# Kernel tuning notes

Measured on AMD Instinct MI355X. Metric: run time of the kernel, lower is better.

The kernel has to match this reference:

```python
import jax, jax.numpy as jnp
import numpy as np
from jax.scipy.special import ndtri

BLOCK_SIZE = 32
NF5_OFFSET = 0.9677083  # QLoRA-style tail quantile offset


def _nf5_table():
    # 32-level NormalFloat-5 table: 16 negative levels, zero, 15 positive levels,
    # taken from standard-normal quantiles and normalized so endpoints hit -1 / +1.
    neg = ndtri(jnp.linspace(1.0 - NF5_OFFSET, 0.5, 17))[:-1]   # 16 negative quantiles
    pos = ndtri(jnp.linspace(0.5, NF5_OFFSET, 16))[1:]          # 15 positive quantiles
    neg = neg / (-neg[0])
    pos = pos / pos[-1]
    return jnp.concatenate([neg, jnp.zeros((1,)), pos]).astype(jnp.float32)


def nf5_quantize(x, block_size, table, boundaries):
    # Block-wise NF5 quantization with power-of-2 scales along the last dim.
    shp = x.shape
    xb = x.reshape(-1, block_size)                               # [nblocks, B]
    amax = jnp.max(jnp.abs(xb), axis=1, keepdims=True)
    scale = jnp.exp2(jnp.ceil(jnp.log2(jnp.maximum(amax, 1e-12))))  # power-of-2 scale
    n = xb / scale                                               # normalized to [-1, 1]
    idx = jnp.searchsorted(boundaries, n)                        # nearest-level index
    q = table[idx] * scale                                       # fused dequant
    return q.reshape(shp)


def setup_inputs() -> dict:
    key = jax.random.key(0)
    k1, k2, k3 = jax.random.split(key, 3)
    B, S, Din, Dout = 8, 4096, 1024, 1024
    x = jax.random.normal(k1, (B, S, Din), dtype=jnp.float32)
    # kaiming_uniform_(a=sqrt(5)) -> U(-b, b) with b = sqrt(6/((1+5)*fan_in)) = 1/sqrt(fan_in)
    bound_w = 1.0 / np.sqrt(Din)
    weight = jax.random.uniform(k2, (Dout, Din), minval=-bound_w, maxval=bound_w, dtype=jnp.float32)
    bias = jax.random.uniform(k3, (Dout,), minval=-bound_w, maxval=bound_w, dtype=jnp.float32)
    return {"x": x, "weight": weight, "bias": bias}


def reference(x, weight, bias):
    table = _nf5_table()
    boundaries = (table[:-1] + table[1:]) * 0.5
    qw = nf5_quantize(weight, BLOCK_SIZE, table, boundaries)   # quantize weight along in_features
    qx = nf5_quantize(x, BLOCK_SIZE, table, boundaries)        # quantize_input=True
    # y[b,s,o] = sum_k qx[b,s,k] * qw[o,k] + bias[o]
    y = jnp.einsum('bsk,ok->bso', qx, qw) + bias
    return y
```

## Files before the change

### kernel.cpp

```cpp
#include <hip/hip_runtime.h>
#include <hip/hip_bf16.h>

typedef __attribute__((ext_vector_type(8))) short short8;
typedef __attribute__((ext_vector_type(4))) float f32x4;

struct alignas(8) US4 { unsigned short x, y, z, w; };

__device__ double ndtri_d(double p) {
    const double a1 = -3.969683028665376e+01, a2 = 2.209460984245205e+02,
                 a3 = -2.759285104469687e+02, a4 = 1.383577518672690e+02,
                 a5 = -3.066479806614716e+01, a6 = 2.506628277459239e+00;
    const double b1 = -5.447609879822406e+01, b2 = 1.615858368580409e+02,
                 b3 = -1.556989798598866e+02, b4 = 6.680131188771972e+01,
                 b5 = -1.328068155288572e+01;
    const double c1 = -7.784894002430293e-03, c2 = -3.223964580411365e-01,
                 c3 = -2.400758277161838e+00, c4 = -2.549732539343734e+00,
                 c5 = 4.374664141464968e+00,  c6 = 2.938163982698783e+00;
    const double d1 = 7.784695709041462e-03, d2 = 3.224671290700398e-01,
                 d3 = 2.445134137142996e+00, d4 = 3.754408661907416e+00;
    const double plow = 0.02425, phigh = 1.0 - 0.02425;
    double x;
    if (p < plow) {
        double q = sqrt(-2.0 * log(p));
        x = (((((c1*q+c2)*q+c3)*q+c4)*q+c5)*q+c6) / ((((d1*q+d2)*q+d3)*q+d4)*q+1.0);
    } else if (p <= phigh) {
        double q = p - 0.5, r = q * q;
        x = (((((a1*r+a2)*r+a3)*r+a4)*r+a5)*r+a6)*q / (((((b1*r+b2)*r+b3)*r+b4)*r+b5)*r+1.0);
    } else {
        double q = sqrt(-2.0 * log(1.0 - p));
        x = -(((((c1*q+c2)*q+c3)*q+c4)*q+c5)*q+c6) / ((((d1*q+d2)*q+d3)*q+d4)*q+1.0);
    }
    #pragma unroll
    for (int it = 0; it < 2; ++it) {
        double e = 0.5 * erfc(-x * 0.70710678118654752440) - p;
        double u = e * 2.50662827463100050242 * exp(0.5 * x * x);
        x = x - u / (1.0 + 0.5 * x * u);
    }
    return x;
}

__global__ void build_table_k(float* __restrict__ table, float* __restrict__ bounds) {
    __shared__ float sT[32];
    const int i = threadIdx.x;
    const double OFF = 0.9677083;
    double v;
    if (i == 16) {
        v = 0.0;
    } else if (i < 16) {
        const double a = 1.0 - OFF;
        double p = a + (0.5 - a) * ((double)i / 16.0);
        v = ndtri_d(p) / (-ndtri_d(a));
    } else {
        int j = i - 16;
        double p = 0.5 + (OFF - 0.5) * ((double)j / 15.0);
        v = ndtri_d(p) / ndtri_d(OFF);
    }
    float tv = (float)v;
    sT[i] = tv;
    table[i] = tv;
    __syncthreads();
    if (i < 31) bounds[i] = 0.5f * (sT[i] + sT[i + 1]);
    else        bounds[31] = __builtin_inff();
}

__device__ __forceinline__ unsigned short q_one(float n, const float* sT,
                                                const float* sB, float scale) {
    int idx = (sB[15] < n) ? 16 : 0;
    idx += (sB[idx + 7] < n) ? 8 : 0;
    idx += (sB[idx + 3] < n) ? 4 : 0;
    idx += (sB[idx + 1] < n) ? 2 : 0;
    idx += (sB[idx]     < n) ? 1 : 0;
    float q = sT[idx] * scale;
    __hip_bfloat16 h = __float2bfloat16(q);
    return *reinterpret_cast<unsigned short*>(&h);
}

__global__ __launch_bounds__(256) void quantize_k(const float4* __restrict__ in,
                                                  US4* __restrict__ out,
                                                  const float* __restrict__ table,
                                                  const float* __restrict__ bounds,
                                                  int n4) {
    __shared__ float sT[32], sB[32];
    const int tid = threadIdx.x;
    if (tid < 32) { sT[tid] = table[tid]; sB[tid] = bounds[tid]; }
    __syncthreads();
    const int t = blockIdx.x * 256 + tid;
    if (t >= n4) return;
    float4 v = in[t];
    float am = fmaxf(fmaxf(fabsf(v.x), fabsf(v.y)), fmaxf(fabsf(v.z), fabsf(v.w)));
    am = fmaxf(am, __shfl_xor(am, 1));
    am = fmaxf(am, __shfl_xor(am, 2));
    am = fmaxf(am, __shfl_xor(am, 4));
    am = fmaxf(am, 1e-12f);
    int e;
    float m = frexpf(am, &e);
    int se = (m == 0.5f) ? (e - 1) : e;
    float scale = ldexpf(1.0f, se);
    float inv   = ldexpf(1.0f, -se);
    US4 o;
    o.x = q_one(v.x * inv, sT, sB, scale);
    o.y = q_one(v.y * inv, sT, sB, scale);
    o.z = q_one(v.z * inv, sT, sB, scale);
    o.w = q_one(v.w * inv, sT, sB, scale);
    out[t] = o;
}

__device__ __forceinline__ void gload_lds16(const unsigned short* g, unsigned short* s) {
    __builtin_amdgcn_global_load_lds(
        (const __attribute__((address_space(1))) unsigned int*)g,
        (__attribute__((address_space(3))) unsigned int*)s, 16, 0, 0);
}

__global__ __launch_bounds__(256) void gemm_bt_k(const unsigned short* __restrict__ A,
                                                 const unsigned short* __restrict__ B,
                                                 const float* __restrict__ bias,
                                                 float* __restrict__ C,
                                                 int M, int N, int K) {
    __shared__ unsigned short sA[128 * 64];
    __shared__ unsigned short sB[128 * 64];
    const int t = threadIdx.x;
    const int w = t >> 6, l = t & 63;
    const int m_blk = blockIdx.y * 128, n_blk = blockIdx.x * 128;
    const int wm = (w >> 1) * 64, wn = (w & 1) * 64;

    f32x4 acc[4][4];
    #pragma unroll
    for (int i = 0; i < 4; ++i)
        #pragma unroll
        for (int j = 0; j < 4; ++j)
            acc[i][j] = (f32x4){0.f, 0.f, 0.f, 0.f};

    const int st_row = (l >> 3);
    const int st_col = (l & 7) * 8;

    for (int kt = 0; kt < K; kt += 64) {
        __syncthreads();
        #pragma unroll
        for (int j = 0; j < 4; ++j) {
            const int chunk = w * 4 + j;
            const int row = chunk * 8 + st_row;
            const unsigned short* ga = A + (size_t)(m_blk + row) * K + kt + st_col;
            const unsigned short* gb = B + (size_t)(n_blk + row) * K + kt + st_col;
            gload_lds16(ga, &sA[chunk * 512]);
            gload_lds16(gb, &sB[chunk * 512]);
        }
        __syncthreads();
        #pragma unroll
        for (int ks = 0; ks < 2; ++ks) {
            const int kof = ks * 32 + (l >> 4) * 8;
            const int rsel = l & 15;
            short8 a[4], b[4];
            #pragma unroll
            for (int i = 0; i < 4; ++i) {
                a[i] = *(const short8*)&sA[(wm + i * 16 + rsel) * 64 + kof];
                b[i] = *(const short8*)&sB[(wn + i * 16 + rsel) * 64 + kof];
            }
            #pragma unroll
            for (int i = 0; i < 4; ++i)
                #pragma unroll
                for (int j = 0; j < 4; ++j)
                    acc[i][j] = __builtin_amdgcn_mfma_f32_16x16x32_bf16(
                        a[i], b[j], acc[i][j], 0, 0, 0);
        }
    }

    float bv[4];
    #pragma unroll
    for (int j = 0; j < 4; ++j) bv[j] = bias[n_blk + wn + j * 16 + (l & 15)];
    #pragma unroll
    for (int i = 0; i < 4; ++i) {
        #pragma unroll
        for (int r = 0; r < 4; ++r) {
            const int row = m_blk + wm + i * 16 + (l >> 4) * 4 + r;
            float* cp = C + (size_t)row * N + n_blk + wn + (l & 15);
            #pragma unroll
            for (int j = 0; j < 4; ++j)
                cp[j * 16] = acc[i][j][r] + bv[j];
        }
    }
}

extern "C" void kernel_launch(void* const* d_in, const int* in_sizes, int n_in,
                              void* d_out, int out_size, void* d_ws, size_t ws_size,
                              hipStream_t stream) {
    const float* x    = (const float*)d_in[0];
    const float* wgt  = (const float*)d_in[1];
    const float* bias = (const float*)d_in[2];
    float* out = (float*)d_out;

    const int x_size = in_sizes[0];
    const int w_size = in_sizes[1];
    const int N = in_sizes[2];
    const int K = w_size / N;
    const int M = x_size / K;

    char* ws = (char*)d_ws;
    unsigned short* qx = (unsigned short*)ws;
    unsigned short* qw = (unsigned short*)(ws + (size_t)M * K * sizeof(unsigned short));
    float* table  = (float*)(ws + (size_t)M * K * 2 + (size_t)N * K * 2);
    float* bounds = table + 32;

    build_table_k<<<1, 32, 0, stream>>>(table, bounds);

    const int n4x = x_size / 4;
    quantize_k<<<(n4x + 255) / 256, 256, 0, stream>>>(
        (const float4*)x, (US4*)qx, table, bounds, n4x);
    const int n4w = w_size / 4;
    quantize_k<<<(n4w + 255) / 256, 256, 0, stream>>>(
        (const float4*)wgt, (US4*)qw, table, bounds, n4w);

    dim3 grid(N / 128, M / 128);
    gemm_bt_k<<<grid, 256, 0, stream>>>(qx, qw, bias, out, M, N, K);
}
```

Baseline: 338.5 us.

## Use LUT-based NF5 quantization, 8 elems per thread, and XCD-aware GEMM tile mapping

Builds a 256-entry lookup table that maps each normalized value bucket to a candidate level index, so the five-step binary search becomes one LUT read plus one boundary compare. Each quantize thread now handles 8 elements with 16-byte stores, and the amax reduction needs one fewer shuffle. The GEMM grid becomes 1D and is remapped so the 8 XCDs get contiguous M rows, aiming for better L2 reuse. The risks are LUT bucket edge cases near the boundaries and a remap that only applies when the M-block count is a multiple of 8.

```diff
diff --git a/kernel.cpp b/kernel.cpp
--- a/kernel.cpp
+++ b/kernel.cpp
@@ -4,7 +4,7 @@
 typedef __attribute__((ext_vector_type(8))) short short8;
 typedef __attribute__((ext_vector_type(4))) float f32x4;
 
-struct alignas(8) US4 { unsigned short x, y, z, w; };
+struct alignas(16) US8 { unsigned short s[8]; };
 
 __device__ double ndtri_d(double p) {
     const double a1 = -3.969683028665376e+01, a2 = 2.209460984245205e+02,
@@ -39,8 +39,9 @@
     return x;
 }
 
-__global__ void build_table_k(float* __restrict__ table, float* __restrict__ bounds) {
-    __shared__ float sT[32];
+__global__ void build_table_k(float* __restrict__ table, float* __restrict__ bounds,
+                              unsigned char* __restrict__ lut) {
+    __shared__ float sT[32], sBd[32];
     const int i = threadIdx.x;
     const double OFF = 0.9677083;
     double v;
@@ -59,49 +60,69 @@
     sT[i] = tv;
     table[i] = tv;
     __syncthreads();
-    if (i < 31) bounds[i] = 0.5f * (sT[i] + sT[i + 1]);
-    else        bounds[31] = __builtin_inff();
-}
-
-__device__ __forceinline__ unsigned short q_one(float n, const float* sT,
-                                                const float* sB, float scale) {
-    int idx = (sB[15] < n) ? 16 : 0;
-    idx += (sB[idx + 7] < n) ? 8 : 0;
-    idx += (sB[idx + 3] < n) ? 4 : 0;
-    idx += (sB[idx + 1] < n) ? 2 : 0;
-    idx += (sB[idx]     < n) ? 1 : 0;
+    float bd;
+    if (i < 31) bd = 0.5f * (sT[i] + sT[i + 1]);
+    else        bd = __builtin_inff();
+    sBd[i] = bd;
+    bounds[i] = bd;
+    __syncthreads();
+    for (int j = i; j < 256; j += 32) {
+        float nj = (float)j * (1.0f / 128.0f) - 1.0f - 0x1p-20f;
+        int c = 0;
+        #pragma unroll
+        for (int k = 0; k < 31; ++k) c += (sBd[k] < nj) ? 1 : 0;
+        lut[j] = (unsigned char)c;
+    }
+}
+
+__device__ __forceinline__ unsigned short q_one(float n, float scale,
+                                                const float* sT, const float* sBnd,
+                                                const unsigned char* sLut) {
+    float u = fmaf(n, 0.5f, 0.5f);
+    int b = (int)(u * 256.0f);
+    b = min(b, 255);
+    int base = sLut[b];
+    int idx = base + ((sBnd[base] < n) ? 1 : 0);
     float q = sT[idx] * scale;
     __hip_bfloat16 h = __float2bfloat16(q);
     return *reinterpret_cast<unsigned short*>(&h);
 }
 
 __global__ __launch_bounds__(256) void quantize_k(const float4* __restrict__ in,
-                                                  US4* __restrict__ out,
+                                                  US8* __restrict__ out,
                                                   const float* __restrict__ table,
                                                   const float* __restrict__ bounds,
-                                                  int n4) {
-    __shared__ float sT[32], sB[32];
+                                                  const unsigned char* __restrict__ lut,
+                                                  int n8) {
+    __shared__ float sT[32], sBnd[32];
+    __shared__ unsigned char sLut[256];
     const int tid = threadIdx.x;
-    if (tid < 32) { sT[tid] = table[tid]; sB[tid] = bounds[tid]; }
+    if (tid < 32) { sT[tid] = table[tid]; sBnd[tid] = bounds[tid]; }
+    sLut[tid] = lut[tid];
     __syncthreads();
     const int t = blockIdx.x * 256 + tid;
-    if (t >= n4) return;
-    float4 v = in[t];
-    float am = fmaxf(fmaxf(fabsf(v.x), fabsf(v.y)), fmaxf(fabsf(v.z), fabsf(v.w)));
+    if (t >= n8) return;
+    float4 v0 = in[2 * t];
+    float4 v1 = in[2 * t + 1];
+    float am = fmaxf(fmaxf(fmaxf(fabsf(v0.x), fabsf(v0.y)), fmaxf(fabsf(v0.z), fabsf(v0.w))),
+                     fmaxf(fmaxf(fabsf(v1.x), fabsf(v1.y)), fmaxf(fabsf(v1.z), fabsf(v1.w))));
     am = fmaxf(am, __shfl_xor(am, 1));
     am = fmaxf(am, __shfl_xor(am, 2));
-    am = fmaxf(am, __shfl_xor(am, 4));
     am = fmaxf(am, 1e-12f);
     int e;
     float m = frexpf(am, &e);
     int se = (m == 0.5f) ? (e - 1) : e;
     float scale = ldexpf(1.0f, se);
     float inv   = ldexpf(1.0f, -se);
-    US4 o;
-    o.x = q_one(v.x * inv, sT, sB, scale);
-    o.y = q_one(v.y * inv, sT, sB, scale);
-    o.z = q_one(v.z * inv, sT, sB, scale);
-    o.w = q_one(v.w * inv, sT, sB, scale);
+    US8 o;
+    o.s[0] = q_one(v0.x * inv, scale, sT, sBnd, sLut);
+    o.s[1] = q_one(v0.y * inv, scale, sT, sBnd, sLut);
+    o.s[2] = q_one(v0.z * inv, scale, sT, sBnd, sLut);
+    o.s[3] = q_one(v0.w * inv, scale, sT, sBnd, sLut);
+    o.s[4] = q_one(v1.x * inv, scale, sT, sBnd, sLut);
+    o.s[5] = q_one(v1.y * inv, scale, sT, sBnd, sLut);
+    o.s[6] = q_one(v1.z * inv, scale, sT, sBnd, sLut);
+    o.s[7] = q_one(v1.w * inv, scale, sT, sBnd, sLut);
     out[t] = o;
 }
 
@@ -120,7 +141,19 @@
     __shared__ unsigned short sB[128 * 64];
     const int t = threadIdx.x;
     const int w = t >> 6, l = t & 63;
-    const int m_blk = blockIdx.y * 128, n_blk = blockIdx.x * 128;
+
+    const int nB = N >> 7, mB = M >> 7;
+    const unsigned int lin = blockIdx.x;
+    int m_idx, n_idx;
+    if ((mB & 7) == 0) {
+        const unsigned int xcd = lin & 7, seq = lin >> 3;
+        n_idx = seq % (unsigned int)nB;
+        m_idx = (seq / (unsigned int)nB) * 8 + xcd;
+    } else {
+        n_idx = lin % (unsigned int)nB;
+        m_idx = lin / (unsigned int)nB;
+    }
+    const int m_blk = m_idx * 128, n_blk = n_idx * 128;
     const int wm = (w >> 1) * 64, wn = (w & 1) * 64;
 
     f32x4 acc[4][4];
@@ -199,16 +232,17 @@
     unsigned short* qw = (unsigned short*)(ws + (size_t)M * K * sizeof(unsigned short));
     float* table  = (float*)(ws + (size_t)M * K * 2 + (size_t)N * K * 2);
     float* bounds = table + 32;
-
-    build_table_k<<<1, 32, 0, stream>>>(table, bounds);
-
-    const int n4x = x_size / 4;
-    quantize_k<<<(n4x + 255) / 256, 256, 0, stream>>>(
-        (const float4*)x, (US4*)qx, table, bounds, n4x);
-    const int n4w = w_size / 4;
-    quantize_k<<<(n4w + 255) / 256, 256, 0, stream>>>(
-        (const float4*)wgt, (US4*)qw, table, bounds, n4w);
-
-    dim3 grid(N / 128, M / 128);
+    unsigned char* lut = (unsigned char*)(bounds + 32);
+
+    build_table_k<<<1, 32, 0, stream>>>(table, bounds, lut);
+
+    const int n8x = x_size / 8;
+    quantize_k<<<(n8x + 255) / 256, 256, 0, stream>>>(
+        (const float4*)x, (US8*)qx, table, bounds, lut, n8x);
+    const int n8w = w_size / 8;
+    quantize_k<<<(n8w + 255) / 256, 256, 0, stream>>>(
+        (const float4*)wgt, (US8*)qw, table, bounds, lut, n8w);
+
+    const int grid = (M / 128) * (N / 128);
     gemm_bt_k<<<grid, 256, 0, stream>>>(qx, qw, bias, out, M, N, K);
 }
```

Result: no change. 334.7 us (-1.1%).
